# Optimization experiments

Hardware: AMD Instinct MI355X
Metric: run time of the kernel (lower is better)

## Reference

```python
import jax, jax.numpy as jnp
import numpy as np

B, NEG = 4, 33          # queries, candidates per query
N, R = 10000, 256       # entities, relation types (even; R//2 direct)
D, L = 64, 6            # hidden dim, conv layers
E, ER = 200000, 80000   # entity edges, edges per relation graph (hh/ht/th/tt)
F = 2 * D
EPS = 1e-5


def _ln(x, s, b):
    m = jnp.mean(x, -1, keepdims=True)
    v = jnp.mean((x - m) ** 2, -1, keepdims=True)
    return (x - m) * jax.lax.rsqrt(v + EPS) * s + b


def _conv(x, boundary, relation, src, dst, etype, p):
    # GeneralizedRelationalConv (dependent=False, project_relations=True):
    # distmult message, sum aggregate + boundary self-loop, update=relu(LN(Linear([x,agg])))
    p1w, p1b, p2w, p2b, lw, lb, lns, lnb = p
    rel = jax.nn.relu(relation @ p1w + p1b) @ p2w + p2b     # relation projection MLP
    msg = x[:, src, :] * rel[:, etype, :]                   # [B, Eg, D] gathered messages
    agg = jnp.zeros_like(boundary).at[:, dst, :].add(msg) + boundary
    out = jnp.concatenate([x, agg], -1) @ lw + lb
    return jax.nn.relu(_ln(out, lns, lnb))


def _entity_bf(rel_reps, h0, r0, src, dst, etype, params):
    # NBFNet Bellman-Ford over the entity graph, query-conditioned boundary
    q = rel_reps[jnp.arange(B), r0]                         # [B, D]
    boundary = jnp.zeros((B, N, D), q.dtype).at[jnp.arange(B), h0].add(q)
    x = boundary
    for i in range(L):
        x = _conv(x, boundary, rel_reps, src, dst, etype,
                  tuple(t[i] for t in params)) + x          # short_cut residual
    nq = jnp.broadcast_to(q[:, None, :], (B, N, D))
    return jnp.concatenate([x, nq], -1)                     # [B, N, 2D]


def _forward(floats, ints):
    (e1p1w, e1p1b, e1p2w, e1p2b, e1lw, e1lb, e1lns, e1lnb,
     e2p1w, e2p1b, e2p2w, e2p2b, e2lw, e2lb, e2lns, e2lnb,
     e2m1w, e2m1b, e2m2w, e2m2b,
     rp1w, rp1b, rp2w, rp2b, rlw, rlb, rlns, rlnb, nmw, nmb) = floats
    edge_src, edge_dst, edge_type, rel_src, rel_dst, rel_etype, batch = ints
    h0 = batch[:, 0, 0]
    t_idx = batch[:, :, 1]
    r0 = batch[:, 0, 2]
    e1p = (e1p1w, e1p1b, e1p2w, e1p2b, e1lw, e1lb, e1lns, e1lnb)
    # ---- RelNet over the 4 relation graphs (nodes=relations, edge types=entities) ----
    node_reps = jnp.ones((B, N, D), e1p1w.dtype)
    q = jnp.ones((B, D), e1p1w.dtype)
    boundary = jnp.zeros((B, R, D), q.dtype).at[jnp.arange(B), r0].add(q)
    x = boundary
    for i in range(L):
        h = sum(_conv(x, boundary, node_reps, rel_src[g], rel_dst[g], rel_etype[g],
                      (rp1w[g, i], rp1b[g, i], rp2w[g, i], rp2b[g, i],
                       rlw[g, i], rlb[g, i], rlns[g, i], rlnb[g, i]))
                for g in range(4))
        x = h + x                                           # short_cut
        if i == 0:
            # entity_model_1 refreshes the per-entity (relation-graph edge type) reps
            feat = _entity_bf(x, h0, r0, edge_src, edge_dst, edge_type, e1p)
            node_reps = feat @ nmw + nmb                    # [B, N, D]
    rel_reps = x                                            # [B, R, D]
    # ---- EntityNet 2: score candidates ----
    e2p = (e2p1w, e2p1b, e2p2w, e2p2b, e2lw, e2lb, e2lns, e2lnb)
    feat2 = _entity_bf(rel_reps, h0, r0, edge_src, edge_dst, edge_type, e2p)
    g = jnp.take_along_axis(feat2, jnp.broadcast_to(t_idx[:, :, None], (B, NEG, F)), axis=1)
    score = (jax.nn.relu(g @ e2m1w + e2m1b) @ e2m2w + e2m2b)[..., 0]
    return score                                            # [B, NEG]


def setup_inputs():
    key = jax.random.key(0)
    ks = iter(jax.random.split(key, 64))
    def w(shape, std=0.08):
        return jax.random.normal(next(ks), shape, jnp.float32) * std
    inp = {}
    inp["edge_src"] = jax.random.randint(next(ks), (E,), 0, N, jnp.int32)
    inp["edge_dst"] = jax.random.randint(next(ks), (E,), 0, N, jnp.int32)
    inp["edge_type"] = jax.random.randint(next(ks), (E,), 0, R, jnp.int32)
    inp["rel_src"] = jax.random.randint(next(ks), (4, ER), 0, R, jnp.int32)
    inp["rel_dst"] = jax.random.randint(next(ks), (4, ER), 0, R, jnp.int32)
    inp["rel_etype"] = jax.random.randint(next(ks), (4, ER), 0, N, jnp.int32)
    h = jax.random.randint(next(ks), (B, 1), 0, N, jnp.int32)
    t = jax.random.randint(next(ks), (B, NEG), 0, N, jnp.int32)
    r = jax.random.randint(next(ks), (B, 1), 0, R // 2, jnp.int32)
    inp["batch"] = jnp.stack([jnp.broadcast_to(h, (B, NEG)), t,
                              jnp.broadcast_to(r, (B, NEG))], -1)
    for pre in ("e1", "e2"):
        inp[pre + "p1w"] = w((L, D, D)); inp[pre + "p1b"] = jnp.zeros((L, D))
        inp[pre + "p2w"] = w((L, D, D)); inp[pre + "p2b"] = jnp.zeros((L, D))
        inp[pre + "lw"] = w((L, F, D));  inp[pre + "lb"] = jnp.zeros((L, D))
        inp[pre + "lns"] = jnp.ones((L, D)); inp[pre + "lnb"] = jnp.zeros((L, D))
    inp["e2m1w"] = w((F, F)); inp["e2m1b"] = jnp.zeros((F,))
    inp["e2m2w"] = w((F, 1)); inp["e2m2b"] = jnp.zeros((1,))
    inp["rp1w"] = w((4, L, D, D)); inp["rp1b"] = jnp.zeros((4, L, D))
    inp["rp2w"] = w((4, L, D, D)); inp["rp2b"] = jnp.zeros((4, L, D))
    inp["rlw"] = w((4, L, F, D));  inp["rlb"] = jnp.zeros((4, L, D))
    inp["rlns"] = jnp.ones((4, L, D)); inp["rlnb"] = jnp.zeros((4, L, D))
    inp["nmw"] = w((F, D)); inp["nmb"] = jnp.zeros((D,))
    return inp


def reference(e1p1w, e1p1b, e1p2w, e1p2b, e1lw, e1lb, e1lns, e1lnb,
              e2p1w, e2p1b, e2p2w, e2p2b, e2lw, e2lb, e2lns, e2lnb,
              e2m1w, e2m1b, e2m2w, e2m2b,
              rp1w, rp1b, rp2w, rp2b, rlw, rlb, rlns, rlnb, nmw, nmb,
              edge_src, edge_dst, edge_type, rel_src, rel_dst, rel_etype, batch):
    floats = (e1p1w, e1p1b, e1p2w, e1p2b, e1lw, e1lb, e1lns, e1lnb,
              e2p1w, e2p1b, e2p2w, e2p2b, e2lw, e2lb, e2lns, e2lnb,
              e2m1w, e2m1b, e2m2w, e2m2b,
              rp1w, rp1b, rp2w, rp2b, rlw, rlb, rlns, rlnb, nmw, nmb)
    ints = (edge_src, edge_dst, edge_type, rel_src, rel_dst, rel_etype, batch)
    return _forward(floats, ints)
```

## Files before the change

### kernel.cpp

```cpp
#include <hip/hip_runtime.h>

constexpr int kB   = 4;
constexpr int kNEG = 33;
constexpr int kN   = 10000;
constexpr int kR   = 256;
constexpr int kD   = 64;
constexpr int kL   = 6;
constexpr int kE   = 200000;
constexpr int kER  = 80000;

typedef const float* fp;
typedef __attribute__((ext_vector_type(8))) short bf16x8;
typedef __attribute__((ext_vector_type(4))) float f32x4;

__device__ __forceinline__ float rdlane(float v, int l) {
  return __uint_as_float(__builtin_amdgcn_readlane(__float_as_uint(v), l));
}
__device__ __forceinline__ float wave_sum64(float v) {
  #pragma unroll
  for (int o = 32; o > 0; o >>= 1) v += __shfl_xor(v, o, 64);
  return v;
}
__device__ __forceinline__ short f2bf(float x) {
  unsigned u = __float_as_uint(x);
  unsigned r = (u + 0x7fffu + ((u >> 16) & 1u)) >> 16;
  return (short)r;
}
__device__ __forceinline__ float bf2f_u(unsigned short s) {
  return __uint_as_float(((unsigned)s) << 16);
}
__device__ __forceinline__ float bf2f(short s) { return bf2f_u((unsigned short)s); }

__global__ void k_fill(float* __restrict__ p, float v, int n) {
  int i = blockIdx.x * blockDim.x + threadIdx.x;
  int stride = gridDim.x * blockDim.x;
  for (; i < n; i += stride) p[i] = v;
}
__global__ void k_zero_i(int* __restrict__ p, int n) {
  int i = blockIdx.x * blockDim.x + threadIdx.x;
  int stride = gridDim.x * blockDim.x;
  for (; i < n; i += stride) p[i] = 0;
}
__global__ void k_add_row(float* __restrict__ dst, const int* __restrict__ batch) {
  int tid = threadIdx.x;
  int b = tid >> 6, d = tid & 63;
  int row = batch[b * kNEG * 3 + 2];
  dst[((size_t)b * kR + row) * 64 + d] += 1.0f;
}
__global__ void k_mirror_relx(const float* __restrict__ rel_x, float* __restrict__ rxi) {
  int i = blockIdx.x * blockDim.x + threadIdx.x;
  int d = i & 63, r = (i >> 6) & 255, b = i >> 14;
  rxi[((size_t)r * 4 + b) * 64 + d] = rel_x[i];
}
__global__ void k_get_q(float* __restrict__ q, const float* __restrict__ relx,
                        const int* __restrict__ batch) {
  int tid = threadIdx.x;
  int b = tid >> 6, d = tid & 63;
  int r0 = batch[b * kNEG * 3 + 2];
  q[b * 64 + d] = relx[((size_t)b * kR + r0) * 64 + d];
}

__global__ void k_hist(const int* __restrict__ dst, int ne, int* __restrict__ cnt) {
  int i = blockIdx.x * blockDim.x + threadIdx.x;
  if (i < ne) atomicAdd(&cnt[dst[i]], 1);
}
__global__ void k_hist_rel(const int* __restrict__ rel_dst, int* __restrict__ cnt) {
  int g = blockIdx.y;
  int i = blockIdx.x * blockDim.x + threadIdx.x;
  if (i < kER) atomicAdd(&cnt[g * 256 + rel_dst[(size_t)g * kER + i]], 1);
}
__global__ void k_scan_multi(const int* __restrict__ cnt, int* __restrict__ start,
                             int* __restrict__ cursor, int n, int cstride, int sstride) {
  const int* c = cnt + (size_t)blockIdx.x * cstride;
  int* st = start + (size_t)blockIdx.x * sstride;
  int* cu = cursor + (size_t)blockIdx.x * sstride;
  __shared__ int part[256];
  int t = threadIdx.x;
  int chunk = (n + 255) / 256;
  int lo = t * chunk, hi = min(lo + chunk, n);
  int s = 0;
  for (int i = lo; i < hi; ++i) s += c[i];
  part[t] = s;
  __syncthreads();
  if (t == 0) { int run = 0; for (int i = 0; i < 256; ++i) { int v = part[i]; part[i] = run; run += v; } }
  __syncthreads();
  int run = part[t];
  for (int i = lo; i < hi; ++i) { st[i] = run; cu[i] = run; run += c[i]; }
  if (t == 255) st[n] = run;
}
__global__ void k_fill_csr(const int* __restrict__ src, const int* __restrict__ dst,
                           const int* __restrict__ et, int ne,
                           int* __restrict__ cursor, int2* __restrict__ out) {
  int i = blockIdx.x * blockDim.x + threadIdx.x;
  if (i < ne) {
    int p = atomicAdd(&cursor[dst[i]], 1);
    out[p] = make_int2(src[i], et[i]);
  }
}
__global__ void k_fill_csr_rel(const int* __restrict__ src, const int* __restrict__ dst,
                               const int* __restrict__ et,
                               int* __restrict__ cursor, int2* __restrict__ out) {
  int g = blockIdx.y;
  int i = blockIdx.x * blockDim.x + threadIdx.x;
  if (i < kER) {
    int p = atomicAdd(&cursor[g * 257 + dst[(size_t)g * kER + i]], 1);
    out[(size_t)g * kER + p] = make_int2(src[(size_t)g * kER + i], et[(size_t)g * kER + i]);
  }
}

__global__ void k_packw(const float* __restrict__ w1, const float* __restrict__ w2,
                        short* __restrict__ w1h, short* __restrict__ w1l,
                        short* __restrict__ w2h, short* __restrict__ w2l) {
  int pg = blockIdx.x;
  for (int i = threadIdx.x; i < 4096; i += 256) {
    int t = i & 7, lane = (i >> 3) & 63, nt = (i >> 9) & 3, ks = i >> 11;
    int mr = lane & 15, kg = lane >> 4;
    int src = pg * 4096 + (ks * 32 + kg * 8 + t) * 64 + nt * 16 + mr;
    int dst = pg * 4096 + i;
    float v1 = w1[src]; short h1 = f2bf(v1);
    w1h[dst] = h1; w1l[dst] = f2bf(v1 - bf2f(h1));
    float v2 = w2[src]; short h2 = f2bf(v2);
    w2h[dst] = h2; w2l[dst] = f2bf(v2 - bf2f(h2));
  }
}

__global__ void __launch_bounds__(256) k_mlp_mfma(
    const float* __restrict__ in, const short* __restrict__ w1h, const short* __restrict__ w1l,
    const float* __restrict__ b1, const short* __restrict__ w2h, const short* __restrict__ w2l,
    const float* __restrict__ b2, int layer, unsigned short* __restrict__ out) {
  int g = blockIdx.y;
  int pg = g * kL + layer;
  int w = threadIdx.x >> 6, lane = threadIdx.x & 63;
  int mrow = lane & 15, kgrp = lane >> 4;
  int r0 = blockIdx.x * 64 + w * 16;
  __shared__ float hbuf[4][16][68];
  const float* xp = in + (size_t)(r0 + mrow) * 64 + kgrp * 8;
  bf16x8 a1h[2], a1l[2];
  #pragma unroll
  for (int ks = 0; ks < 2; ++ks) {
    #pragma unroll
    for (int t = 0; t < 8; ++t) {
      float v = xp[ks * 32 + t];
      short h = f2bf(v); a1h[ks][t] = h; a1l[ks][t] = f2bf(v - bf2f(h));
    }
  }
  const bf16x8* B1h = (const bf16x8*)(w1h + (size_t)pg * 4096);
  const bf16x8* B1l = (const bf16x8*)(w1l + (size_t)pg * 4096);
  #pragma unroll
  for (int nt = 0; nt < 4; ++nt) {
    f32x4 c = {0.f, 0.f, 0.f, 0.f};
    #pragma unroll
    for (int ks = 0; ks < 2; ++ks) {
      bf16x8 bh = B1h[(ks * 4 + nt) * 64 + lane];
      bf16x8 bl = B1l[(ks * 4 + nt) * 64 + lane];
      c = __builtin_amdgcn_mfma_f32_16x16x32_bf16(a1h[ks], bh, c, 0, 0, 0);
      c = __builtin_amdgcn_mfma_f32_16x16x32_bf16(a1h[ks], bl, c, 0, 0, 0);
      c = __builtin_amdgcn_mfma_f32_16x16x32_bf16(a1l[ks], bh, c, 0, 0, 0);
    }
    int col = nt * 16 + mrow;
    float bv = b1[pg * 64 + col];
    #pragma unroll
    for (int rg = 0; rg < 4; ++rg)
      hbuf[w][kgrp * 4 + rg][col] = fmaxf(c[rg] + bv, 0.f);
  }
  __syncthreads();
  bf16x8 a2h[2], a2l[2];
  #pragma unroll
  for (int ks = 0; ks < 2; ++ks) {
    #pragma unroll
    for (int t = 0; t < 8; ++t) {
      float v = hbuf[w][mrow][ks * 32 + kgrp * 8 + t];
      short h = f2bf(v); a2h[ks][t] = h; a2l[ks][t] = f2bf(v - bf2f(h));
    }
  }
  const bf16x8* B2h = (const bf16x8*)(w2h + (size_t)pg * 4096);
  const bf16x8* B2l = (const bf16x8*)(w2l + (size_t)pg * 4096);
  unsigned short* ob = out + (size_t)g * kB * kN * 64;
  #pragma unroll
  for (int nt = 0; nt < 4; ++nt) {
    f32x4 c = {0.f, 0.f, 0.f, 0.f};
    #pragma unroll
    for (int ks = 0; ks < 2; ++ks) {
      bf16x8 bh = B2h[(ks * 4 + nt) * 64 + lane];
      bf16x8 bl = B2l[(ks * 4 + nt) * 64 + lane];
      c = __builtin_amdgcn_mfma_f32_16x16x32_bf16(a2h[ks], bh, c, 0, 0, 0);
      c = __builtin_amdgcn_mfma_f32_16x16x32_bf16(a2h[ks], bl, c, 0, 0, 0);
      c = __builtin_amdgcn_mfma_f32_16x16x32_bf16(a2l[ks], bh, c, 0, 0, 0);
    }
    int col = nt * 16 + mrow;
    float bv = b2[pg * 64 + col];
    #pragma unroll
    for (int rg = 0; rg < 4; ++rg) {
      int grow = r0 + kgrp * 4 + rg;
      int bb = grow / kN;
      int nn = grow - bb * kN;
      ob[((size_t)nn * 4 + bb) * 64 + col] = (unsigned short)f2bf(c[rg] + bv);
    }
  }
}

__global__ void __launch_bounds__(256) k_mlp_rel6(
    const float* __restrict__ in, fp p1w, fp p1b, fp p2w, fp p2b,
    unsigned short* __restrict__ out) {
  int j = blockIdx.y;
  int row = blockIdx.x * 4 + (threadIdx.x >> 6);
  int lane = threadIdx.x & 63;
  fp W1 = p1w + (size_t)j * 4096;
  fp W2 = p2w + (size_t)j * 4096;
  float xv = in[(size_t)row * 64 + lane];
  float a = p1b[j * 64 + lane];
  float wbuf[8];
  #pragma unroll
  for (int kk = 0; kk < 64; kk += 8) {
    #pragma unroll
    for (int u = 0; u < 8; ++u) wbuf[u] = W1[(kk + u) * 64 + lane];
    #pragma unroll
    for (int u = 0; u < 8; ++u) a = fmaf(rdlane(xv, kk + u), wbuf[u], a);
  }
  a = fmaxf(a, 0.f);
  float c = p2b[j * 64 + lane];
  #pragma unroll
  for (int kk = 0; kk < 64; kk += 8) {
    #pragma unroll
    for (int u = 0; u < 8; ++u) wbuf[u] = W2[(kk + u) * 64 + lane];
    #pragma unroll
    for (int u = 0; u < 8; ++u) c = fmaf(rdlane(a, kk + u), wbuf[u], c);
  }
  int b = row >> 8, r = row & 255;
  out[(((size_t)j * kR + r) * 4 + b) * 64 + lane] = (unsigned short)f2bf(c);
}

__global__ void k_gate0(fp p1w, fp p1b, fp p2w, fp p2b, float* __restrict__ gate0) {
  int g = threadIdx.x >> 6, lane = threadIdx.x & 63;
  int pg = g * kL;
  float a = p1b[pg * 64 + lane];
  #pragma unroll
  for (int k = 0; k < 64; ++k) a += p1w[(size_t)pg * 4096 + k * 64 + lane];
  a = fmaxf(a, 0.f);
  float c = p2b[pg * 64 + lane];
  #pragma unroll
  for (int k = 0; k < 64; ++k)
    c = fmaf(rdlane(a, k), p2w[(size_t)pg * 4096 + k * 64 + lane], c);
  gate0[g * 64 + lane] = c;
}
__global__ void k_rel_agg0(const int* __restrict__ rel_start, const int2* __restrict__ rel_edges,
                           const int* __restrict__ batch, const float* __restrict__ gate0,
                           float* __restrict__ agg) {
  int wid = (blockIdx.x * blockDim.x + threadIdx.x) >> 6;
  int lane = threadIdx.x & 63;
  int g = wid >> 10, rem = wid & 1023, b = rem >> 8, r = rem & 255;
  int r0 = batch[b * kNEG * 3 + 2];
  const int* start = rel_start + g * 257;
  const int2* edges = rel_edges + (size_t)g * kER;
  int s0 = start[r], s1 = start[r + 1];
  int cnt = 0;
  for (int base = s0; base < s1; base += 64) {
    int e = base + lane;
    bool m = false;
    if (e < s1) m = (edges[e].x == r0);
    cnt += (int)__popcll(__ballot(m));
  }
  agg[(size_t)wid * 64 + lane] = gate0[g * 64 + lane] * (float)cnt + ((r == r0) ? 1.f : 0.f);
}

__global__ void __launch_bounds__(256) k_gather_rel_all(
    const float* __restrict__ rxi, const unsigned short* __restrict__ gateN,
    const int* __restrict__ rel_start, const int2* __restrict__ rel_edges,
    const int* __restrict__ batch, float* __restrict__ agg) {
  int i = blockIdx.x;
  int g = i & 3, r = i >> 2;
  const unsigned short* gate = gateN + (size_t)g * kB * kN * 64;
  const int* start = rel_start + g * 257;
  const int2* edges = rel_edges + (size_t)g * kER;
  int w = threadIdx.x >> 6, lane = threadIdx.x & 63;
  int s0 = start[r], s1 = start[r + 1];
  int len = s1 - s0;
  int per = (len + 3) >> 2;
  int e0 = s0 + w * per, e1 = min(e0 + per, s1);
  float a0 = 0.f, a1 = 0.f, a2 = 0.f, a3 = 0.f;
  int2 se;
  if (e0 < e1) se = edges[e0];
  for (int e = e0; e < e1; ++e) {
    int2 cur = se;
    if (e + 1 < e1) se = edges[e + 1];
    const float* xp = rxi + (size_t)cur.x * 256 + lane;
    const unsigned short* gp = gate + (size_t)cur.y * 256 + lane;
    a0 = fmaf(xp[0],   bf2f_u(gp[0]),   a0);
    a1 = fmaf(xp[64],  bf2f_u(gp[64]),  a1);
    a2 = fmaf(xp[128], bf2f_u(gp[128]), a2);
    a3 = fmaf(xp[192], bf2f_u(gp[192]), a3);
  }
  __shared__ float red[4][4][64];
  red[w][0][lane] = a0; red[w][1][lane] = a1; red[w][2][lane] = a2; red[w][3][lane] = a3;
  __syncthreads();
  float a = red[0][w][lane] + red[1][w][lane] + red[2][w][lane] + red[3][w][lane];
  int r0b = batch[w * kNEG * 3 + 2];
  if (r == r0b) a += 1.0f;
  agg[(((size_t)g * kB + w) * kR + r) * 64 + lane] = a;
}

__global__ void __launch_bounds__(256) k_conv_rel2(
    float* __restrict__ rel_x, float* __restrict__ rxi, const float* __restrict__ agg,
    fp rlw, fp rlb, fp rlns, fp rlnb, int layer) {
  int row = blockIdx.x;
  int g = threadIdx.x >> 6, lane = threadIdx.x & 63;
  int pg = g * kL + layer;
  float xr = rel_x[(size_t)row * 64 + lane];
  float ag = agg[((size_t)g * kB * kR + row) * 64 + lane];
  fp w1 = rlw + (size_t)pg * 8192;
  float o = rlb[pg * 64 + lane];
  float wbuf[8];
  #pragma unroll
  for (int kk = 0; kk < 128; kk += 8) {
    #pragma unroll
    for (int u = 0; u < 8; ++u) wbuf[u] = w1[(kk + u) * 64 + lane];
    #pragma unroll
    for (int u = 0; u < 8; ++u) {
      int k = kk + u;
      float xv = (k < 64) ? rdlane(xr, k) : rdlane(ag, k - 64);
      o = fmaf(xv, wbuf[u], o);
    }
  }
  float m = wave_sum64(o) * (1.f / 64.f);
  float c = o - m;
  float v = wave_sum64(c * c) * (1.f / 64.f);
  float y = fmaxf(c * rsqrtf(v + 1e-5f) * rlns[pg * 64 + lane] + rlnb[pg * 64 + lane], 0.f);
  __shared__ float red[4][64];
  red[g][lane] = y;
  __syncthreads();
  if (g == 0) {
    float newx = xr + red[0][lane] + red[1][lane] + red[2][lane] + red[3][lane];
    rel_x[(size_t)row * 64 + lane] = newx;
    int b = row >> 8, r = row & 255;
    rxi[((size_t)r * 4 + b) * 64 + lane] = newx;
  }
}

template<bool FIRST>
__global__ void __launch_bounds__(256) k_ent_layer2(
    const float* __restrict__ xcur, float* __restrict__ xnext,
    const unsigned short* __restrict__ xbf_cur, unsigned short* __restrict__ xbf_next,
    const unsigned short* __restrict__ gateL,
    const int* __restrict__ start, const int2* __restrict__ edges,
    const float* __restrict__ q, const int* __restrict__ batch,
    fp lw, fp lb, fp lns, fp lnb) {
  int n = (blockIdx.x * blockDim.x + threadIdx.x) >> 6;
  if (n >= kN) return;
  int lane = threadIdx.x & 63;
  int h0[4]; float qv[4];
  #pragma unroll
  for (int b = 0; b < 4; ++b) { h0[b] = batch[b * kNEG * 3]; qv[b] = q[b * 64 + lane]; }
  float a0 = 0.f, a1 = 0.f, a2 = 0.f, a3 = 0.f;
  int s0 = start[n], s1 = start[n + 1];
  int2 se;
  if (s0 < s1) se = edges[s0];
  for (int e = s0; e < s1; ++e) {
    int2 cur = se;
    if (e + 1 < s1) se = edges[e + 1];
    const unsigned short* gp = gateL + (size_t)cur.y * 256 + lane;
    if (FIRST) {
      if (cur.x == h0[0]) a0 = fmaf(qv[0], bf2f_u(gp[0]),   a0);
      if (cur.x == h0[1]) a1 = fmaf(qv[1], bf2f_u(gp[64]),  a1);
      if (cur.x == h0[2]) a2 = fmaf(qv[2], bf2f_u(gp[128]), a2);
      if (cur.x == h0[3]) a3 = fmaf(qv[3], bf2f_u(gp[192]), a3);
    } else {
      const unsigned short* xp = xbf_cur + (size_t)cur.x * 256 + lane;
      a0 = fmaf(bf2f_u(xp[0]),   bf2f_u(gp[0]),   a0);
      a1 = fmaf(bf2f_u(xp[64]),  bf2f_u(gp[64]),  a1);
      a2 = fmaf(bf2f_u(xp[128]), bf2f_u(gp[128]), a2);
      a3 = fmaf(bf2f_u(xp[192]), bf2f_u(gp[192]), a3);
    }
  }
  if (n == h0[0]) a0 += qv[0];
  if (n == h0[1]) a1 += qv[1];
  if (n == h0[2]) a2 += qv[2];
  if (n == h0[3]) a3 += qv[3];
  float x0, x1, x2, x3;
  if (FIRST) {
    x0 = (n == h0[0]) ? qv[0] : 0.f; x1 = (n == h0[1]) ? qv[1] : 0.f;
    x2 = (n == h0[2]) ? qv[2] : 0.f; x3 = (n == h0[3]) ? qv[3] : 0.f;
  } else {
    const float* xp = xcur + (size_t)n * 64 + lane;
    x0 = xp[0]; x1 = xp[640000]; x2 = xp[1280000]; x3 = xp[1920000];
  }
  float bv = lb[lane];
  float o0 = bv, o1 = bv, o2 = bv, o3 = bv;
  float wbuf[8];
  #pragma unroll
  for (int kk = 0; kk < 128; kk += 8) {
    #pragma unroll
    for (int u = 0; u < 8; ++u) wbuf[u] = lw[(kk + u) * 64 + lane];
    #pragma unroll
    for (int u = 0; u < 8; ++u) {
      int k = kk + u; float w = wbuf[u];
      if (k < 64) {
        o0 = fmaf(rdlane(x0, k), w, o0); o1 = fmaf(rdlane(x1, k), w, o1);
        o2 = fmaf(rdlane(x2, k), w, o2); o3 = fmaf(rdlane(x3, k), w, o3);
      } else {
        o0 = fmaf(rdlane(a0, k - 64), w, o0); o1 = fmaf(rdlane(a1, k - 64), w, o1);
        o2 = fmaf(rdlane(a2, k - 64), w, o2); o3 = fmaf(rdlane(a3, k - 64), w, o3);
      }
    }
  }
  float s = lns[lane], t = lnb[lane];
  float* yp = xnext + (size_t)n * 64 + lane;
  unsigned short* mp = xbf_next + (size_t)n * 256 + lane;
  { float m = wave_sum64(o0) * (1.f/64.f); float c = o0 - m;
    float v = wave_sum64(c*c) * (1.f/64.f);
    float y = x0 + fmaxf(c * rsqrtf(v + 1e-5f) * s + t, 0.f);
    yp[0] = y; mp[0] = (unsigned short)f2bf(y); }
  { float m = wave_sum64(o1) * (1.f/64.f); float c = o1 - m;
    float v = wave_sum64(c*c) * (1.f/64.f);
    float y = x1 + fmaxf(c * rsqrtf(v + 1e-5f) * s + t, 0.f);
    yp[640000] = y; mp[64] = (unsigned short)f2bf(y); }
  { float m = wave_sum64(o2) * (1.f/64.f); float c = o2 - m;
    float v = wave_sum64(c*c) * (1.f/64.f);
    float y = x2 + fmaxf(c * rsqrtf(v + 1e-5f) * s + t, 0.f);
    yp[1280000] = y; mp[128] = (unsigned short)f2bf(y); }
  { float m = wave_sum64(o3) * (1.f/64.f); float c = o3 - m;
    float v = wave_sum64(c*c) * (1.f/64.f);
    float y = x3 + fmaxf(c * rsqrtf(v + 1e-5f) * s + t, 0.f);
    yp[1920000] = y; mp[192] = (unsigned short)f2bf(y); }
}

__global__ void __launch_bounds__(256) k_nodeup4(
    const float* __restrict__ x, const float* __restrict__ q,
    fp nmw, fp nmb, float* __restrict__ out) {
  int wid = (blockIdx.x * blockDim.x + threadIdx.x) >> 6;
  int lane = threadIdx.x & 63;
  int r0 = wid * 4;
  if (r0 >= kB * kN) return;
  int b = r0 / kN;
  const float* ip = x + (size_t)r0 * 64 + lane;
  float x0 = ip[0], x1 = ip[64], x2 = ip[128], x3 = ip[192];
  float qv = q[b * 64 + lane];
  float bv = nmb[lane];
  float c0 = bv, c1 = bv, c2 = bv, c3 = bv;
  float wbuf[4];
  #pragma unroll
  for (int kk = 0; kk < 64; kk += 4) {
    #pragma unroll
    for (int u = 0; u < 4; ++u) wbuf[u] = nmw[(kk + u) * 64 + lane];
    #pragma unroll
    for (int u = 0; u < 4; ++u) {
      int k = kk + u; float w = wbuf[u];
      c0 = fmaf(rdlane(x0, k), w, c0); c1 = fmaf(rdlane(x1, k), w, c1);
      c2 = fmaf(rdlane(x2, k), w, c2); c3 = fmaf(rdlane(x3, k), w, c3);
    }
  }
  float qa = 0.f;
  #pragma unroll
  for (int k = 0; k < 64; ++k)
    qa = fmaf(rdlane(qv, k), nmw[(64 + k) * 64 + lane], qa);
  float* op = out + (size_t)r0 * 64 + lane;
  op[0] = c0 + qa; op[64] = c1 + qa; op[128] = c2 + qa; op[192] = c3 + qa;
}

__global__ void k_score(const float* __restrict__ entx, const float* __restrict__ q,
                        const int* __restrict__ batch,
                        fp m1w, fp m1b, fp m2w, fp m2b,
                        float* __restrict__ out) {
  int b = blockIdx.x / kNEG, n = blockIdx.x % kNEG;
  int t = batch[(b * kNEG + n) * 3 + 1];
  int j = threadIdx.x;
  __shared__ float gv[128];
  __shared__ float red[2];
  gv[j] = (j < 64) ? entx[((size_t)b * kN + t) * 64 + j] : q[b * 64 + (j - 64)];
  __syncthreads();
  float acc = m1b[j];
  #pragma unroll 16
  for (int k = 0; k < 128; ++k)
    acc = fmaf(gv[k], m1w[k * 128 + j], acc);
  float h = fmaxf(acc, 0.f) * m2w[j];
  h = wave_sum64(h);
  if ((j & 63) == 0) red[j >> 6] = h;
  __syncthreads();
  if (j == 0) out[b * kNEG + n] = red[0] + red[1] + m2b[0];
}

extern "C" void kernel_launch(void* const* d_in, const int* in_sizes, int n_in,
                              void* d_out, int out_size, void* d_ws, size_t ws_size,
                              hipStream_t stream) {
  const int* edge_src  = (const int*)d_in[0];
  const int* edge_dst  = (const int*)d_in[1];
  const int* edge_type = (const int*)d_in[2];
  const int* rel_src   = (const int*)d_in[3];
  const int* rel_dst   = (const int*)d_in[4];
  const int* rel_etype = (const int*)d_in[5];
  const int* batch     = (const int*)d_in[6];
  fp e1p1w = (fp)d_in[7],  e1p1b = (fp)d_in[8],  e1p2w = (fp)d_in[9],  e1p2b = (fp)d_in[10];
  fp e1lw  = (fp)d_in[11], e1lb  = (fp)d_in[12], e1lns = (fp)d_in[13], e1lnb = (fp)d_in[14];
  fp e2p1w = (fp)d_in[15], e2p1b = (fp)d_in[16], e2p2w = (fp)d_in[17], e2p2b = (fp)d_in[18];
  fp e2lw  = (fp)d_in[19], e2lb  = (fp)d_in[20], e2lns = (fp)d_in[21], e2lnb = (fp)d_in[22];
  fp e2m1w = (fp)d_in[23], e2m1b = (fp)d_in[24], e2m2w = (fp)d_in[25], e2m2b = (fp)d_in[26];
  fp rp1w  = (fp)d_in[27], rp1b  = (fp)d_in[28], rp2w  = (fp)d_in[29], rp2b  = (fp)d_in[30];
  fp rlw   = (fp)d_in[31], rlb   = (fp)d_in[32], rlns  = (fp)d_in[33], rlnb  = (fp)d_in[34];
  fp nmw   = (fp)d_in[35], nmb   = (fp)d_in[36];

  float* ws = (float*)d_ws;
  float* rel_x     = ws;
  float* q         = rel_x + 65536;
  float* gate0     = q + 256;
  float* rxi       = gate0 + 256;
  float* rel_agg   = rxi + 65536;
  float* node_reps = rel_agg + 262144;
  float* ent_xa    = node_reps + 2560000;
  float* ent_xb    = ent_xa + 2560000;
  unsigned short* gateR6 = (unsigned short*)(ent_xb + 2560000);
  unsigned short* gateN  = gateR6 + 393216;
  unsigned short* ent_ba = gateN + 10240000;
  unsigned short* ent_bb = ent_ba + 2560000;
  int*   iws       = (int*)(ent_bb + 2560000);
  int2*  ent_edges = (int2*)iws;
  int2*  rel_edges = (int2*)(iws + 400000);
  int*   ent_cnt   = iws + 400000 + 640000;
  int*   ent_start = ent_cnt + 10000;
  int*   ent_cur   = ent_start + 10001;
  int*   rel_cnt   = ent_cur + 10001;
  int*   rel_start = rel_cnt + 1024;
  int*   rel_cur   = rel_start + 1028;
  short* w1hp      = (short*)(rel_cur + 1028 + 2);
  short* w1lp      = w1hp + 98304;
  short* w2hp      = w1lp + 98304;
  short* w2lp      = w2hp + 98304;

  const int nZero = 10000 + 10001 + 10001 + 1024;
  k_zero_i<<<(nZero + 255) / 256, 256, 0, stream>>>(ent_cnt, nZero);
  k_hist<<<(kE + 255) / 256, 256, 0, stream>>>(edge_dst, kE, ent_cnt);
  k_hist_rel<<<dim3((kER + 255) / 256, 4), 256, 0, stream>>>(rel_dst, rel_cnt);
  k_scan_multi<<<1, 256, 0, stream>>>(ent_cnt, ent_start, ent_cur, 10000, 0, 0);
  k_scan_multi<<<4, 256, 0, stream>>>(rel_cnt, rel_start, rel_cur, 256, 256, 257);
  k_fill_csr<<<(kE + 255) / 256, 256, 0, stream>>>(edge_src, edge_dst, edge_type, kE, ent_cur, ent_edges);
  k_fill_csr_rel<<<dim3((kER + 255) / 256, 4), 256, 0, stream>>>(rel_src, rel_dst, rel_etype, rel_cur, rel_edges);
  k_packw<<<24, 256, 0, stream>>>(rp1w, rp2w, w1hp, w1lp, w2hp, w2lp);

  k_fill<<<256, 256, 0, stream>>>(rel_x, 0.f, kB * kR * kD);
  k_add_row<<<1, 256, 0, stream>>>(rel_x, batch);

  k_gate0<<<1, 256, 0, stream>>>(rp1w, rp1b, rp2w, rp2b, gate0);
  k_rel_agg0<<<1024, 256, 0, stream>>>(rel_start, rel_edges, batch, gate0, rel_agg);
  k_conv_rel2<<<1024, 256, 0, stream>>>(rel_x, rxi, rel_agg, rlw, rlb, rlns, rlnb, 0);

  k_get_q<<<1, 256, 0, stream>>>(q, rel_x, batch);
  k_mlp_rel6<<<dim3(256, 6), 256, 0, stream>>>(rel_x, e1p1w, e1p1b, e1p2w, e1p2b, gateR6);
  {
    float* cur = ent_xa; float* nxt = ent_xb;
    unsigned short* bcur = ent_ba; unsigned short* bnxt = ent_bb;
    for (int j = 0; j < kL; ++j) {
      const unsigned short* gL = gateR6 + (size_t)j * kR * 4 * 64;
      if (j == 0)
        k_ent_layer2<true><<<2500, 256, 0, stream>>>(cur, nxt, bcur, bnxt, gL, ent_start, ent_edges, q, batch,
            e1lw + (size_t)j * 8192, e1lb + (size_t)j * 64, e1lns + (size_t)j * 64, e1lnb + (size_t)j * 64);
      else
        k_ent_layer2<false><<<2500, 256, 0, stream>>>(cur, nxt, bcur, bnxt, gL, ent_start, ent_edges, q, batch,
            e1lw + (size_t)j * 8192, e1lb + (size_t)j * 64, e1lns + (size_t)j * 64, e1lnb + (size_t)j * 64);
      float* tf = cur; cur = nxt; nxt = tf;
      unsigned short* tb = bcur; bcur = bnxt; bnxt = tb;
    }
    k_nodeup4<<<2500, 256, 0, stream>>>(cur, q, nmw, nmb, node_reps);
  }

  for (int i = 1; i < kL; ++i) {
    k_mlp_mfma<<<dim3(625, 4), 256, 0, stream>>>(node_reps, w1hp, w1lp, rp1b, w2hp, w2lp, rp2b, i, gateN);
    k_gather_rel_all<<<1024, 256, 0, stream>>>(rxi, gateN, rel_start, rel_edges, batch, rel_agg);
    k_conv_rel2<<<1024, 256, 0, stream>>>(rel_x, rxi, rel_agg, rlw, rlb, rlns, rlnb, i);
  }

  k_get_q<<<1, 256, 0, stream>>>(q, rel_x, batch);
  k_mlp_rel6<<<dim3(256, 6), 256, 0, stream>>>(rel_x, e2p1w, e2p1b, e2p2w, e2p2b, gateR6);
  {
    float* cur = ent_xa; float* nxt = ent_xb;
    unsigned short* bcur = ent_ba; unsigned short* bnxt = ent_bb;
    for (int j = 0; j < kL; ++j) {
      const unsigned short* gL = gateR6 + (size_t)j * kR * 4 * 64;
      if (j == 0)
        k_ent_layer2<true><<<2500, 256, 0, stream>>>(cur, nxt, bcur, bnxt, gL, ent_start, ent_edges, q, batch,
            e2lw + (size_t)j * 8192, e2lb + (size_t)j * 64, e2lns + (size_t)j * 64, e2lnb + (size_t)j * 64);
      else
        k_ent_layer2<false><<<2500, 256, 0, stream>>>(cur, nxt, bcur, bnxt, gL, ent_start, ent_edges, q, batch,
            e2lw + (size_t)j * 8192, e2lb + (size_t)j * 64, e2lns + (size_t)j * 64, e2lnb + (size_t)j * 64);
      float* tf = cur; cur = nxt; nxt = tf;
      unsigned short* tb = bcur; bcur = bnxt; bnxt = tb;
    }
    k_score<<<kB * kNEG, 128, 0, stream>>>(cur, q, batch, e2m1w, e2m1b, e2m2w, e2m2b, (float*)d_out);
  }
}
```

Baseline: 1.054 ms.

## Use LDS-privatized CSR build and restructure relation conv for weight reuse

The CSR histogram and fill kernels now count edges in shared-memory bins per block and reserve global ranges with one atomic per bin, replacing one global atomic per edge. The relation conv kernel now has each wave process four rows against one loaded weight column, and the cross-graph sum moves to a separate k_sum_rel kernel that writes rel_x and rxi. This is meant to cut global atomic contention and redundant weight loads. In exchange it adds an extra launch per layer and leaves only 16 blocks for the entity CSR build, which limits parallelism. Edge order within a bin changes, which can reorder floating-point sums.

```diff
diff --git a/kernel.cpp b/kernel.cpp
--- a/kernel.cpp
+++ b/kernel.cpp
@@ -47,11 +47,6 @@
   int row = batch[b * kNEG * 3 + 2];
   dst[((size_t)b * kR + row) * 64 + d] += 1.0f;
 }
-__global__ void k_mirror_relx(const float* __restrict__ rel_x, float* __restrict__ rxi) {
-  int i = blockIdx.x * blockDim.x + threadIdx.x;
-  int d = i & 63, r = (i >> 6) & 255, b = i >> 14;
-  rxi[((size_t)r * 4 + b) * 64 + d] = rel_x[i];
-}
 __global__ void k_get_q(float* __restrict__ q, const float* __restrict__ relx,
                         const int* __restrict__ batch) {
   int tid = threadIdx.x;
@@ -60,14 +55,71 @@
   q[b * 64 + d] = relx[((size_t)b * kR + r0) * 64 + d];
 }
 
-__global__ void k_hist(const int* __restrict__ dst, int ne, int* __restrict__ cnt) {
-  int i = blockIdx.x * blockDim.x + threadIdx.x;
-  if (i < ne) atomicAdd(&cnt[dst[i]], 1);
-}
-__global__ void k_hist_rel(const int* __restrict__ rel_dst, int* __restrict__ cnt) {
+__global__ void k_hist_rel_lds(const int* __restrict__ rel_dst, int* __restrict__ cnt) {
   int g = blockIdx.y;
-  int i = blockIdx.x * blockDim.x + threadIdx.x;
-  if (i < kER) atomicAdd(&cnt[g * 256 + rel_dst[(size_t)g * kER + i]], 1);
+  __shared__ int lc[256];
+  lc[threadIdx.x] = 0;
+  __syncthreads();
+  int lo = blockIdx.x * 8000, hi = min(lo + 8000, kER);
+  for (int e = lo + threadIdx.x; e < hi; e += 256)
+    atomicAdd(&lc[rel_dst[(size_t)g * kER + e]], 1);
+  __syncthreads();
+  int c = lc[threadIdx.x];
+  if (c) atomicAdd(&cnt[g * 256 + threadIdx.x], c);
+}
+__global__ void k_fill_rel_lds(const int* __restrict__ src, const int* __restrict__ dst,
+                               const int* __restrict__ et,
+                               int* __restrict__ cursor, int2* __restrict__ out) {
+  int g = blockIdx.y;
+  __shared__ int lc[256];
+  lc[threadIdx.x] = 0;
+  __syncthreads();
+  int lo = blockIdx.x * 8000, hi = min(lo + 8000, kER);
+  const int* db = dst + (size_t)g * kER;
+  for (int e = lo + threadIdx.x; e < hi; e += 256)
+    atomicAdd(&lc[db[e]], 1);
+  __syncthreads();
+  int c = lc[threadIdx.x];
+  __syncthreads();
+  lc[threadIdx.x] = c ? atomicAdd(&cursor[g * 257 + threadIdx.x], c) : 0;
+  __syncthreads();
+  for (int e = lo + threadIdx.x; e < hi; e += 256) {
+    int bin = db[e];
+    int p = atomicAdd(&lc[bin], 1);
+    out[(size_t)g * kER + p] = make_int2(src[(size_t)g * kER + e], et[(size_t)g * kER + e]);
+  }
+}
+__global__ void k_hist_ent_lds(const int* __restrict__ dst, int* __restrict__ cnt) {
+  __shared__ int lc[10000];
+  for (int i = threadIdx.x; i < 10000; i += 256) lc[i] = 0;
+  __syncthreads();
+  int lo = blockIdx.x * 12500, hi = min(lo + 12500, kE);
+  for (int e = lo + threadIdx.x; e < hi; e += 256)
+    atomicAdd(&lc[dst[e]], 1);
+  __syncthreads();
+  for (int i = threadIdx.x; i < 10000; i += 256)
+    if (lc[i]) atomicAdd(&cnt[i], lc[i]);
+}
+__global__ void k_fill_ent_lds(const int* __restrict__ src, const int* __restrict__ dst,
+                               const int* __restrict__ et,
+                               int* __restrict__ cursor, int2* __restrict__ out) {
+  __shared__ int lc[10000];
+  for (int i = threadIdx.x; i < 10000; i += 256) lc[i] = 0;
+  __syncthreads();
+  int lo = blockIdx.x * 12500, hi = min(lo + 12500, kE);
+  for (int e = lo + threadIdx.x; e < hi; e += 256)
+    atomicAdd(&lc[dst[e]], 1);
+  __syncthreads();
+  for (int i = threadIdx.x; i < 10000; i += 256) {
+    int c = lc[i];
+    lc[i] = c ? atomicAdd(&cursor[i], c) : 0;
+  }
+  __syncthreads();
+  for (int e = lo + threadIdx.x; e < hi; e += 256) {
+    int bin = dst[e];
+    int p = atomicAdd(&lc[bin], 1);
+    out[p] = make_int2(src[e], et[e]);
+  }
 }
 __global__ void k_scan_multi(const int* __restrict__ cnt, int* __restrict__ start,
                              int* __restrict__ cursor, int n, int cstride, int sstride) {
@@ -87,25 +139,6 @@
   int run = part[t];
   for (int i = lo; i < hi; ++i) { st[i] = run; cu[i] = run; run += c[i]; }
   if (t == 255) st[n] = run;
-}
-__global__ void k_fill_csr(const int* __restrict__ src, const int* __restrict__ dst,
-                           const int* __restrict__ et, int ne,
-                           int* __restrict__ cursor, int2* __restrict__ out) {
-  int i = blockIdx.x * blockDim.x + threadIdx.x;
-  if (i < ne) {
-    int p = atomicAdd(&cursor[dst[i]], 1);
-    out[p] = make_int2(src[i], et[i]);
-  }
-}
-__global__ void k_fill_csr_rel(const int* __restrict__ src, const int* __restrict__ dst,
-                               const int* __restrict__ et,
-                               int* __restrict__ cursor, int2* __restrict__ out) {
-  int g = blockIdx.y;
-  int i = blockIdx.x * blockDim.x + threadIdx.x;
-  if (i < kER) {
-    int p = atomicAdd(&cursor[g * 257 + dst[(size_t)g * kER + i]], 1);
-    out[(size_t)g * kER + p] = make_int2(src[(size_t)g * kER + i], et[(size_t)g * kER + i]);
-  }
 }
 
 __global__ void k_packw(const float* __restrict__ w1, const float* __restrict__ w2,
@@ -299,16 +332,20 @@
   agg[(((size_t)g * kB + w) * kR + r) * 64 + lane] = a;
 }
 
-__global__ void __launch_bounds__(256) k_conv_rel2(
-    float* __restrict__ rel_x, float* __restrict__ rxi, const float* __restrict__ agg,
+__global__ void __launch_bounds__(256) k_conv_rel3(
+    const float* __restrict__ rel_x, float* __restrict__ agg,
     fp rlw, fp rlb, fp rlns, fp rlnb, int layer) {
-  int row = blockIdx.x;
-  int g = threadIdx.x >> 6, lane = threadIdx.x & 63;
+  int g = blockIdx.y;
   int pg = g * kL + layer;
-  float xr = rel_x[(size_t)row * 64 + lane];
-  float ag = agg[((size_t)g * kB * kR + row) * 64 + lane];
+  int wave = threadIdx.x >> 6, lane = threadIdx.x & 63;
+  int row0 = blockIdx.x * 16 + wave * 4;
+  const float* xp = rel_x + (size_t)row0 * 64 + lane;
+  float* ap = agg + ((size_t)g * 1024 + row0) * 64 + lane;
+  float x0 = xp[0], x1 = xp[64], x2 = xp[128], x3 = xp[192];
+  float g0 = ap[0], g1 = ap[64], g2 = ap[128], g3 = ap[192];
   fp w1 = rlw + (size_t)pg * 8192;
-  float o = rlb[pg * 64 + lane];
+  float bv = rlb[pg * 64 + lane];
+  float o0 = bv, o1 = bv, o2 = bv, o3 = bv;
   float wbuf[8];
   #pragma unroll
   for (int kk = 0; kk < 128; kk += 8) {
@@ -316,24 +353,39 @@
     for (int u = 0; u < 8; ++u) wbuf[u] = w1[(kk + u) * 64 + lane];
     #pragma unroll
     for (int u = 0; u < 8; ++u) {
-      int k = kk + u;
-      float xv = (k < 64) ? rdlane(xr, k) : rdlane(ag, k - 64);
-      o = fmaf(xv, wbuf[u], o);
-    }
-  }
-  float m = wave_sum64(o) * (1.f / 64.f);
-  float c = o - m;
-  float v = wave_sum64(c * c) * (1.f / 64.f);
-  float y = fmaxf(c * rsqrtf(v + 1e-5f) * rlns[pg * 64 + lane] + rlnb[pg * 64 + lane], 0.f);
-  __shared__ float red[4][64];
-  red[g][lane] = y;
-  __syncthreads();
-  if (g == 0) {
-    float newx = xr + red[0][lane] + red[1][lane] + red[2][lane] + red[3][lane];
-    rel_x[(size_t)row * 64 + lane] = newx;
-    int b = row >> 8, r = row & 255;
-    rxi[((size_t)r * 4 + b) * 64 + lane] = newx;
-  }
+      int k = kk + u; float w = wbuf[u];
+      if (k < 64) {
+        o0 = fmaf(rdlane(x0, k), w, o0); o1 = fmaf(rdlane(x1, k), w, o1);
+        o2 = fmaf(rdlane(x2, k), w, o2); o3 = fmaf(rdlane(x3, k), w, o3);
+      } else {
+        o0 = fmaf(rdlane(g0, k - 64), w, o0); o1 = fmaf(rdlane(g1, k - 64), w, o1);
+        o2 = fmaf(rdlane(g2, k - 64), w, o2); o3 = fmaf(rdlane(g3, k - 64), w, o3);
+      }
+    }
+  }
+  float s = rlns[pg * 64 + lane], t = rlnb[pg * 64 + lane];
+  { float m = wave_sum64(o0) * (1.f/64.f); float c = o0 - m;
+    float v = wave_sum64(c*c) * (1.f/64.f);
+    ap[0] = fmaxf(c * rsqrtf(v + 1e-5f) * s + t, 0.f); }
+  { float m = wave_sum64(o1) * (1.f/64.f); float c = o1 - m;
+    float v = wave_sum64(c*c) * (1.f/64.f);
+    ap[64] = fmaxf(c * rsqrtf(v + 1e-5f) * s + t, 0.f); }
+  { float m = wave_sum64(o2) * (1.f/64.f); float c = o2 - m;
+    float v = wave_sum64(c*c) * (1.f/64.f);
+    ap[128] = fmaxf(c * rsqrtf(v + 1e-5f) * s + t, 0.f); }
+  { float m = wave_sum64(o3) * (1.f/64.f); float c = o3 - m;
+    float v = wave_sum64(c*c) * (1.f/64.f);
+    ap[192] = fmaxf(c * rsqrtf(v + 1e-5f) * s + t, 0.f); }
+}
+
+__global__ void k_sum_rel(float* __restrict__ rel_x, float* __restrict__ rxi,
+                          const float* __restrict__ y) {
+  int i = blockIdx.x * blockDim.x + threadIdx.x;
+  float v = rel_x[i] + y[i] + y[65536 + i] + y[131072 + i] + y[196608 + i];
+  rel_x[i] = v;
+  int d = i & 63, row = i >> 6;
+  int b = row >> 8, r = row & 255;
+  rxi[(((size_t)r * 4 + b) << 6) + d] = v;
 }
 
 template<bool FIRST>
@@ -526,12 +578,12 @@
 
   const int nZero = 10000 + 10001 + 10001 + 1024;
   k_zero_i<<<(nZero + 255) / 256, 256, 0, stream>>>(ent_cnt, nZero);
-  k_hist<<<(kE + 255) / 256, 256, 0, stream>>>(edge_dst, kE, ent_cnt);
-  k_hist_rel<<<dim3((kER + 255) / 256, 4), 256, 0, stream>>>(rel_dst, rel_cnt);
+  k_hist_ent_lds<<<16, 256, 0, stream>>>(edge_dst, ent_cnt);
+  k_hist_rel_lds<<<dim3(10, 4), 256, 0, stream>>>(rel_dst, rel_cnt);
   k_scan_multi<<<1, 256, 0, stream>>>(ent_cnt, ent_start, ent_cur, 10000, 0, 0);
   k_scan_multi<<<4, 256, 0, stream>>>(rel_cnt, rel_start, rel_cur, 256, 256, 257);
-  k_fill_csr<<<(kE + 255) / 256, 256, 0, stream>>>(edge_src, edge_dst, edge_type, kE, ent_cur, ent_edges);
-  k_fill_csr_rel<<<dim3((kER + 255) / 256, 4), 256, 0, stream>>>(rel_src, rel_dst, rel_etype, rel_cur, rel_edges);
+  k_fill_ent_lds<<<16, 256, 0, stream>>>(edge_src, edge_dst, edge_type, ent_cur, ent_edges);
+  k_fill_rel_lds<<<dim3(10, 4), 256, 0, stream>>>(rel_src, rel_dst, rel_etype, rel_cur, rel_edges);
   k_packw<<<24, 256, 0, stream>>>(rp1w, rp2w, w1hp, w1lp, w2hp, w2lp);
 
   k_fill<<<256, 256, 0, stream>>>(rel_x, 0.f, kB * kR * kD);
@@ -539,7 +591,8 @@
 
   k_gate0<<<1, 256, 0, stream>>>(rp1w, rp1b, rp2w, rp2b, gate0);
   k_rel_agg0<<<1024, 256, 0, stream>>>(rel_start, rel_edges, batch, gate0, rel_agg);
-  k_conv_rel2<<<1024, 256, 0, stream>>>(rel_x, rxi, rel_agg, rlw, rlb, rlns, rlnb, 0);
+  k_conv_rel3<<<dim3(64, 4), 256, 0, stream>>>(rel_x, rel_agg, rlw, rlb, rlns, rlnb, 0);
+  k_sum_rel<<<256, 256, 0, stream>>>(rel_x, rxi, rel_agg);
 
   k_get_q<<<1, 256, 0, stream>>>(q, rel_x, batch);
   k_mlp_rel6<<<dim3(256, 6), 256, 0, stream>>>(rel_x, e1p1w, e1p1b, e1p2w, e1p2b, gateR6);
@@ -563,7 +616,8 @@
   for (int i = 1; i < kL; ++i) {
     k_mlp_mfma<<<dim3(625, 4), 256, 0, stream>>>(node_reps, w1hp, w1lp, rp1b, w2hp, w2lp, rp2b, i, gateN);
     k_gather_rel_all<<<1024, 256, 0, stream>>>(rxi, gateN, rel_start, rel_edges, batch, rel_agg);
-    k_conv_rel2<<<1024, 256, 0, stream>>>(rel_x, rxi, rel_agg, rlw, rlb, rlns, rlnb, i);
+    k_conv_rel3<<<dim3(64, 4), 256, 0, stream>>>(rel_x, rel_agg, rlw, rlb, rlns, rlnb, i);
+    k_sum_rel<<<256, 256, 0, stream>>>(rel_x, rxi, rel_agg);
   }
 
   k_get_q<<<1, 256, 0, stream>>>(q, rel_x, batch);
```

After: 1.013 ms. 3.8% less time.
